# Kernel tuning notes

Hardware: AMD Instinct MI355X
Metric: run time of the kernel (lower is better)

Reference implementation:

```python
import jax, jax.numpy as jnp
import numpy as np

NU = 60000   # num_users
NI = 40000   # num_items
N = NU + NI  # num_nodes
E = 2000000  # num_edges
F = 128      # feat_dim (user_feat_dim == item_feat_dim)
H = 128      # hidden_dim


def setup_inputs() -> dict:
    key = jax.random.key(0)
    ks = jax.random.split(key, 14)
    s = 0.05
    inp = {
        "x": jax.random.normal(ks[0], (N, F), jnp.float32),
        "edge_index": jax.random.randint(ks[1], (2, E), 0, N, dtype=jnp.int32),
        "node_type": jnp.concatenate([jnp.zeros(NU, jnp.int32), jnp.ones(NI, jnp.int32)]),
        # input projections (Linear stores weight as (out, in))
        "w_user": s * jax.random.normal(ks[2], (H, F), jnp.float32),
        "b_user": jnp.zeros((H,), jnp.float32),
        "w_item": s * jax.random.normal(ks[3], (H, F), jnp.float32),
        "b_item": jnp.zeros((H,), jnp.float32),
        # SAGEConv layer 0: lin_l (aggregated neighbors, with bias), lin_r (root, no bias)
        "w_l0": s * jax.random.normal(ks[4], (H, H), jnp.float32),
        "b_l0": s * jax.random.normal(ks[5], (H,), jnp.float32),
        "w_r0": s * jax.random.normal(ks[6], (H, H), jnp.float32),
        # SAGEConv layer 1
        "w_l1": s * jax.random.normal(ks[7], (H, H), jnp.float32),
        "b_l1": s * jax.random.normal(ks[8], (H,), jnp.float32),
        "w_r1": s * jax.random.normal(ks[9], (H, H), jnp.float32),
    }
    return inp


def _sage_conv(h, src, dst, w_l, b_l, w_r):
    # gather source features, max-aggregate onto destinations (PyG aggr='max')
    msg = h[src]                                          # [E, H]
    agg = jax.ops.segment_max(msg, dst, num_segments=N)   # [N, H], -inf where no in-edges
    agg = jnp.where(jnp.isneginf(agg), 0.0, agg)          # PyG fills empty segments with 0
    return agg @ w_l.T + b_l + h @ w_r.T


def reference(x, edge_index, node_type, w_user, b_user, w_item, b_item,
              w_l0, b_l0, w_r0, w_l1, b_l1, w_r1):
    # node_type is sorted: first NU rows are users, rest are items
    src, dst = edge_index[0], edge_index[1]
    user_h = x[:NU] @ w_user.T + b_user                   # [NU, H]
    item_h = x[NU:] @ w_item.T + b_item                   # [NI, H]
    h = jnp.concatenate([user_h, item_h], axis=0)         # [N, H]
    # layer 0 with residual (dims match) then ReLU; dropout is identity in eval
    h = h + _sage_conv(h, src, dst, w_l0, b_l0, w_r0)
    h = jax.nn.relu(h)
    # layer 1 with residual (no activation after last layer)
    h = h + _sage_conv(h, src, dst, w_l1, b_l1, w_r1)
    return (h[:NU], h[NU:])
```

## Files before the change

### kernel.cpp

```cpp
#include <hip/hip_runtime.h>

#define NUSR 60000
#define NITM 40000
#define NN   100000
#define EE   2000000
#define HD   128

#define BW   512
#define NB   196
#define EPB  8192

using bf16x8   = __attribute__((ext_vector_type(8))) short;
using f32x4    = __attribute__((ext_vector_type(4))) float;
using ushort4t = __attribute__((ext_vector_type(4))) unsigned short;
using ushort2t = __attribute__((ext_vector_type(2))) unsigned short;
using ushort8t = __attribute__((ext_vector_type(8))) unsigned short;
using uint4t   = __attribute__((ext_vector_type(4))) unsigned int;

__device__ __forceinline__ unsigned short f2bf(float f) {
    unsigned int u = __float_as_uint(f);
    u += 0x7FFFu + ((u >> 16) & 1u);
    return (unsigned short)(u >> 16);
}
__device__ __forceinline__ float bf2f(unsigned short s) {
    return __uint_as_float(((unsigned int)s) << 16);
}
__device__ __forceinline__ unsigned short keyof(unsigned short b) {
    return (b & 0x8000u) ? (unsigned short)~b : (unsigned short)(b | 0x8000u);
}
__device__ __forceinline__ unsigned unkey32(unsigned k) {
    unsigned negsel = (~k & 0x80008000u) >> 15;
    return k ^ (0x80008000u | (negsel * 0x7FFFu));
}
__device__ __forceinline__ int swz(int row, int col) {
    return row * HD + (col ^ ((row & 7) << 3));
}
__device__ __forceinline__ ushort8t pkmax8(ushort8t a, ushort8t b) {
    return __builtin_elementwise_max(a, b);
}

__global__ __launch_bounds__(256) void bhist_k(const int* __restrict__ dst,
                                               int* __restrict__ bcnt) {
    __shared__ int h[NB];
    int t = threadIdx.x;
    if (t < NB) h[t] = 0;
    __syncthreads();
    int e0 = blockIdx.x * EPB;
    #pragma unroll 4
    for (int i = t; i < EPB; i += 256) {
        int e = e0 + i;
        if (e < EE) atomicAdd(&h[dst[e] >> 9], 1);
    }
    __syncthreads();
    if (t < NB && h[t]) atomicAdd(&bcnt[t], h[t]);
}

__global__ void bscan_k(const int* __restrict__ bcnt, int* __restrict__ bbase,
                        int* __restrict__ bcur, int* __restrict__ off) {
    __shared__ int s[256];
    int t = threadIdx.x;
    int v = (t < NB) ? bcnt[t] : 0;
    s[t] = v;
    __syncthreads();
    for (int d = 1; d < 256; d <<= 1) {
        int a = (t >= d) ? s[t - d] : 0;
        __syncthreads();
        s[t] += a;
        __syncthreads();
    }
    if (t < NB) { bbase[t] = s[t] - v; bcur[t] = s[t] - v; }
    if (t == NB - 1) { bbase[NB] = s[t]; off[NN] = EE; }
}

__global__ __launch_bounds__(256) void bscatter_k(const int* __restrict__ src,
                                                  const int* __restrict__ dst,
                                                  int* __restrict__ bcur,
                                                  unsigned int* __restrict__ bedge) {
    __shared__ int h[NB], base[NB];
    int t = threadIdx.x;
    if (t < NB) h[t] = 0;
    __syncthreads();
    int e0 = blockIdx.x * EPB;
    #pragma unroll 4
    for (int i = t; i < EPB; i += 256) {
        int e = e0 + i;
        if (e < EE) atomicAdd(&h[dst[e] >> 9], 1);
    }
    __syncthreads();
    if (t < NB) {
        int c = h[t];
        base[t] = c ? atomicAdd(&bcur[t], c) : 0;
        h[t] = 0;
    }
    __syncthreads();
    #pragma unroll 4
    for (int i = t; i < EPB; i += 256) {
        int e = e0 + i;
        if (e < EE) {
            int d = dst[e];
            int b = d >> 9;
            int p = base[b] + atomicAdd(&h[b], 1);
            bedge[p] = ((unsigned)(d - (b << 9)) << 17) | (unsigned)src[e];
        }
    }
}

__global__ __launch_bounds__(512) void bcsr_k(const unsigned int* __restrict__ bedge,
                                              const int* __restrict__ bbase,
                                              int* __restrict__ off,
                                              int* __restrict__ csr) {
    __shared__ int cnt[BW], cur[BW], sc[BW];
    int b = blockIdx.x, t = threadIdx.x;
    int n0 = b * BW;
    int nloc = min(BW, NN - n0);
    cnt[t] = 0;
    __syncthreads();
    int e0 = bbase[b], e1 = bbase[b + 1];
    for (int e = e0 + t; e < e1; e += 512)
        atomicAdd(&cnt[bedge[e] >> 17], 1);
    __syncthreads();
    int v = cnt[t];
    sc[t] = v;
    __syncthreads();
    for (int d = 1; d < BW; d <<= 1) {
        int a = (t >= d) ? sc[t - d] : 0;
        __syncthreads();
        sc[t] += a;
        __syncthreads();
    }
    int excl = sc[t] - v;
    if (t < nloc) { off[n0 + t] = e0 + excl; cur[t] = e0 + excl; }
    __syncthreads();
    for (int e = e0 + t; e < e1; e += 512) {
        unsigned ed = bedge[e];
        int p = atomicAdd(&cur[ed >> 17], 1);
        csr[p] = (int)(ed & 0x1FFFFu);
    }
}

__global__ void cvt6i_k(const float* __restrict__ a0, const float* __restrict__ a1,
                        const float* __restrict__ a2, const float* __restrict__ a3,
                        const float* __restrict__ a4, const float* __restrict__ a5,
                        unsigned short* __restrict__ out) {
    int i = blockIdx.x * 256 + threadIdx.x;
    int m = i >> 14, idx = i & 16383;
    const float* s;
    switch (m) {
        case 0: s = a0; break; case 1: s = a1; break; case 2: s = a2; break;
        case 3: s = a3; break; case 4: s = a4; break; default: s = a5; break;
    }
    float v = s[idx];
    if ((m == 3 || m == 5) && (idx >> 7) == (idx & 127)) v += 1.0f;
    out[i] = f2bf(v);
}

__global__ __launch_bounds__(256) void proj_mfma_k(
    const float* __restrict__ x, const unsigned short* __restrict__ wb,
    const float* __restrict__ bias, unsigned short* __restrict__ hkey,
    int row_base, int nrows) {
    __shared__ unsigned short lw[HD * HD];
    int tid = threadIdx.x;
    #pragma unroll
    for (int it = 0; it < 16; ++it) {
        int flat = (it * 256 + tid) * 4;
        int row = flat >> 7, col = flat & 127;
        *(ushort4t*)&lw[swz(row, col)] = *(const ushort4t*)(wb + flat);
    }
    __syncthreads();
    int lane = tid & 63, w = tid >> 6;
    int l15 = lane & 15, l4 = lane >> 4;
    int m0 = blockIdx.x * 128 + w * 32;
    f32x4 acc[2][8] = {};
    #pragma unroll
    for (int kb = 0; kb < 4; ++kb) {
        bf16x8 a[2];
        #pragma unroll
        for (int rt = 0; rt < 2; ++rt) {
            int r = m0 + rt * 16 + l15;
            if (r >= nrows) r = nrows - 1;
            const float* ap = x + (size_t)(row_base + r) * HD + kb * 32 + l4 * 8;
            f32x4 v0 = *(const f32x4*)ap;
            f32x4 v1 = *(const f32x4*)(ap + 4);
            bf16x8 f;
            #pragma unroll
            for (int j = 0; j < 4; ++j) { f[j] = (short)f2bf(v0[j]); f[j + 4] = (short)f2bf(v1[j]); }
            a[rt] = f;
        }
        #pragma unroll
        for (int ct = 0; ct < 8; ++ct) {
            bf16x8 b = *(const bf16x8*)&lw[swz(ct * 16 + l15, kb * 32 + l4 * 8)];
            acc[0][ct] = __builtin_amdgcn_mfma_f32_16x16x32_bf16(a[0], b, acc[0][ct], 0, 0, 0);
            acc[1][ct] = __builtin_amdgcn_mfma_f32_16x16x32_bf16(a[1], b, acc[1][ct], 0, 0, 0);
        }
    }
    __syncthreads();
    #pragma unroll
    for (int ct = 0; ct < 8; ++ct) {
        int col = ct * 16 + l15;
        float bv = bias[col];
        #pragma unroll
        for (int rt = 0; rt < 2; ++rt)
            #pragma unroll
            for (int j = 0; j < 4; ++j) {
                int lrow = w * 32 + rt * 16 + l4 * 4 + j;
                lw[lrow * HD + ((col + ((lrow & 15) << 3)) & 127)] =
                    keyof(f2bf(acc[rt][ct][j] + bv));
            }
    }
    __syncthreads();
    int row = tid >> 1, cb = (tid & 1) * 64;
    int r = blockIdx.x * 128 + row;
    if (r < nrows) {
        int sof = (row & 15) << 3;
        #pragma unroll
        for (int gg = 0; gg < 8; ++gg) {
            uint4t v = *(const uint4t*)&lw[row * HD + ((cb + gg * 8 + sof) & 127)];
            *(uint4t*)(hkey + (size_t)(row_base + r) * HD + cb + gg * 8) = v;
        }
    }
}

__global__ __launch_bounds__(256) void agg_key_k(
    const uint4t* __restrict__ hkey4,
    const int* __restrict__ off, const int* __restrict__ csr,
    uint4t* __restrict__ agg4) {
    int node = (blockIdx.x * 256 + threadIdx.x) >> 6;
    int lane = threadIdx.x & 63;
    if (node >= NN) return;
    int s0 = off[node], s1 = off[node + 1];
    int deg = s1 - s0;
    int q = lane >> 4, l16 = lane & 15;
    ushort8t m = {0, 0, 0, 0, 0, 0, 0, 0};
    int cval = (lane < deg) ? csr[s0 + lane] : 0;
    int nslots = deg < 64 ? deg : 64;
    int niter = (nslots + 3) >> 2;
    for (int u = 0; u < niter; ++u) {
        int idx = u * 4 + q;
        int r = __shfl(cval, idx, 64);
        if (idx < nslots) {
            uint4t v = hkey4[(size_t)r * 16 + l16];
            m = pkmax8(m, *(ushort8t*)&v);
        }
    }
    for (int base = s0 + 64; base < s1; base += 32) {
        #pragma unroll
        for (int u = 0; u < 8; ++u) {
            int jj = base + u * 4 + q;
            if (jj < s1) {
                int r = csr[jj];
                uint4t v = hkey4[(size_t)r * 16 + l16];
                m = pkmax8(m, *(ushort8t*)&v);
            }
        }
    }
    uint4t mu = *(uint4t*)&m;
    #pragma unroll
    for (int c = 0; c < 4; ++c) {
        unsigned a = mu[c];
        unsigned b = (unsigned)__shfl_xor((int)a, 16, 64);
        ushort2t pa = *(ushort2t*)&a, pb = *(ushort2t*)&b;
        pa = __builtin_elementwise_max(pa, pb);
        a = *(unsigned*)&pa;
        b = (unsigned)__shfl_xor((int)a, 32, 64);
        pb = *(ushort2t*)&b;
        pa = __builtin_elementwise_max(pa, pb);
        mu[c] = *(unsigned*)&pa;
    }
    if (q == 0) {
        uint4t outv = {0, 0, 0, 0};
        if (deg > 0) {
            #pragma unroll
            for (int c = 0; c < 4; ++c) outv[c] = unkey32(mu[c]);
        }
        agg4[(size_t)node * 16 + l16] = outv;
    }
}

__global__ __launch_bounds__(512) void combine_mfma_k(
    const unsigned short* __restrict__ hkey, const unsigned short* __restrict__ aggb,
    const unsigned short* __restrict__ wlb, const float* __restrict__ bl,
    const unsigned short* __restrict__ wrb,
    unsigned short* __restrict__ hkey_out, float* __restrict__ fout, int relu) {
    __shared__ unsigned short lw[2][HD * HD];
    int tid = threadIdx.x;
    #pragma unroll
    for (int it = 0; it < 8; ++it) {
        int flat = (it * 512 + tid) * 4;
        int row = flat >> 7, col = flat & 127;
        *(ushort4t*)&lw[0][swz(row, col)] = *(const ushort4t*)(wlb + flat);
        *(ushort4t*)&lw[1][swz(row, col)] = *(const ushort4t*)(wrb + flat);
    }
    __syncthreads();
    int lane = tid & 63, w = tid >> 6;
    int l15 = lane & 15, l4 = lane >> 4;
    int m0 = blockIdx.x * 256 + w * 32;
    const uint4t* hk4 = (const uint4t*)hkey;
    f32x4 acc[2][8] = {};
    #pragma unroll
    for (int kb = 0; kb < 4; ++kb) {
        bf16x8 a1[2], a2[2];
        #pragma unroll
        for (int rt = 0; rt < 2; ++rt) {
            int r = m0 + rt * 16 + l15;
            if (r >= NN) r = NN - 1;
            size_t o = (size_t)r * HD + kb * 32 + l4 * 8;
            a1[rt] = *(const bf16x8*)(aggb + o);
            uint4t aw = hk4[(size_t)r * 16 + kb * 4 + l4];
            bf16x8 f;
            #pragma unroll
            for (int u = 0; u < 4; ++u) {
                unsigned d = unkey32(aw[u]);
                f[2 * u]     = (short)(d & 0xFFFFu);
                f[2 * u + 1] = (short)(d >> 16);
            }
            a2[rt] = f;
        }
        #pragma unroll
        for (int ct = 0; ct < 8; ++ct) {
            bf16x8 b1 = *(const bf16x8*)&lw[0][swz(ct * 16 + l15, kb * 32 + l4 * 8)];
            bf16x8 b2 = *(const bf16x8*)&lw[1][swz(ct * 16 + l15, kb * 32 + l4 * 8)];
            acc[0][ct] = __builtin_amdgcn_mfma_f32_16x16x32_bf16(a1[0], b1, acc[0][ct], 0, 0, 0);
            acc[0][ct] = __builtin_amdgcn_mfma_f32_16x16x32_bf16(a2[0], b2, acc[0][ct], 0, 0, 0);
            acc[1][ct] = __builtin_amdgcn_mfma_f32_16x16x32_bf16(a1[1], b1, acc[1][ct], 0, 0, 0);
            acc[1][ct] = __builtin_amdgcn_mfma_f32_16x16x32_bf16(a2[1], b2, acc[1][ct], 0, 0, 0);
        }
    }
    __syncthreads();
    float* cs = (float*)lw;
    for (int p = 0; p < 2; ++p) {
        if ((w >> 2) == p) {
            #pragma unroll
            for (int ct = 0; ct < 8; ++ct)
                #pragma unroll
                for (int rt = 0; rt < 2; ++rt)
                    #pragma unroll
                    for (int j = 0; j < 4; ++j) {
                        int lrow = (w & 3) * 32 + rt * 16 + l4 * 4 + j;
                        int col = ct * 16 + l15;
                        cs[lrow * HD + ((col + lrow * 4) & 127)] = acc[rt][ct][j];
                    }
        }
        __syncthreads();
        int lrow = tid >> 2, cq = (tid & 3) * 32;
        int r = blockIdx.x * 256 + p * 128 + lrow;
        if (r < NN) {
            const float* crow = cs + lrow * HD;
            int rot = lrow * 4;
            #pragma unroll
            for (int gg = 0; gg < 4; ++gg) {
                int c0 = cq + gg * 8;
                f32x4 cv0 = *(const f32x4*)&crow[(c0 + rot) & 127];
                f32x4 cv1 = *(const f32x4*)&crow[(c0 + 4 + rot) & 127];
                f32x4 bv0 = *(const f32x4*)(bl + c0);
                f32x4 bv1 = *(const f32x4*)(bl + c0 + 4);
                float v[8];
                #pragma unroll
                for (int u = 0; u < 4; ++u) { v[u] = cv0[u] + bv0[u]; v[u + 4] = cv1[u] + bv1[u]; }
                if (relu) {
                    #pragma unroll
                    for (int u = 0; u < 8; ++u) v[u] = fmaxf(v[u], 0.0f);
                }
                if (fout) {
                    f32x4 o0 = {v[0], v[1], v[2], v[3]};
                    f32x4 o1 = {v[4], v[5], v[6], v[7]};
                    *(f32x4*)(fout + (size_t)r * HD + c0) = o0;
                    *(f32x4*)(fout + (size_t)r * HD + c0 + 4) = o1;
                } else {
                    uint4t ov;
                    #pragma unroll
                    for (int u = 0; u < 4; ++u)
                        ov[u] = (unsigned)keyof(f2bf(v[2 * u]))
                              | ((unsigned)keyof(f2bf(v[2 * u + 1])) << 16);
                    *(uint4t*)(hkey_out + (size_t)r * HD + c0) = ov;
                }
            }
        }
        __syncthreads();
    }
}

extern "C" void kernel_launch(void* const* d_in, const int* in_sizes, int n_in,
                              void* d_out, int out_size, void* d_ws, size_t ws_size,
                              hipStream_t stream) {
    const float* x      = (const float*)d_in[0];
    const int*   ei     = (const int*)d_in[1];
    const float* w_user = (const float*)d_in[3];
    const float* b_user = (const float*)d_in[4];
    const float* w_item = (const float*)d_in[5];
    const float* b_item = (const float*)d_in[6];
    const float* w_l0   = (const float*)d_in[7];
    const float* b_l0   = (const float*)d_in[8];
    const float* w_r0   = (const float*)d_in[9];
    const float* w_l1   = (const float*)d_in[10];
    const float* b_l1   = (const float*)d_in[11];
    const float* w_r1   = (const float*)d_in[12];

    const int* e_src = ei;
    const int* e_dst = ei + EE;

    char* ws = (char*)d_ws;
    size_t cur_off = 0;
    auto carve = [&](size_t bytes) {
        void* p = ws + cur_off;
        cur_off = (cur_off + bytes + 255) & ~(size_t)255;
        return p;
    };
    unsigned short* hkey0 = (unsigned short*)carve((size_t)NN * HD * 2);
    unsigned short* hkey1 = (unsigned short*)carve((size_t)NN * HD * 2);
    unsigned short* aggb  = (unsigned short*)carve((size_t)NN * HD * 2);
    unsigned short* wb    = (unsigned short*)carve((size_t)6 * HD * HD * 2);
    int*      off   = (int*)carve((size_t)(NN + 1) * 4);
    int*      csr   = (int*)carve((size_t)EE * 4);
    unsigned* bedge = (unsigned*)carve((size_t)EE * 4);
    int*      bcnt  = (int*)carve((NB + 1) * 4);
    int*      bbase = (int*)carve((NB + 1) * 4);
    int*      bcur  = (int*)carve((NB + 1) * 4);
    (void)ws_size;

    hipMemsetAsync(bcnt, 0, (size_t)NB * 4, stream);
    int nbB = (EE + EPB - 1) / EPB;
    bhist_k<<<nbB, 256, 0, stream>>>(e_dst, bcnt);
    bscan_k<<<1, 256, 0, stream>>>(bcnt, bbase, bcur, off);
    bscatter_k<<<nbB, 256, 0, stream>>>(e_src, e_dst, bcur, bedge);
    bcsr_k<<<NB, 512, 0, stream>>>(bedge, bbase, off, csr);

    cvt6i_k<<<(6 * HD * HD) / 256, 256, 0, stream>>>(w_user, w_item, w_l0, w_r0, w_l1, w_r1, wb);

    proj_mfma_k<<<(NUSR + 127) / 128, 256, 0, stream>>>(x, wb,         b_user, hkey0, 0,    NUSR);
    proj_mfma_k<<<(NITM + 127) / 128, 256, 0, stream>>>(x, wb + 16384, b_item, hkey0, NUSR, NITM);

    agg_key_k<<<NN / 4, 256, 0, stream>>>((const uint4t*)hkey0, off, csr, (uint4t*)aggb);
    combine_mfma_k<<<(NN + 255) / 256, 512, 0, stream>>>(
        hkey0, aggb, wb + 2 * 16384, b_l0, wb + 3 * 16384, hkey1, nullptr, 1);

    agg_key_k<<<NN / 4, 256, 0, stream>>>((const uint4t*)hkey1, off, csr, (uint4t*)aggb);
    combine_mfma_k<<<(NN + 255) / 256, 512, 0, stream>>>(
        hkey1, aggb, wb + 4 * 16384, b_l1, wb + 5 * 16384, nullptr, (float*)d_out, 0);
}
```

Before: 305.4 us.

## Precompute per-block bucket offsets and write fp32 output directly from MFMA registers

The histogram kernel now saves each block's per-bucket counts, and a new per-bucket prefix kernel turns them into exact per-block write bases. The scatter kernel therefore no longer re-reads dst to rebuild the histogram or takes global atomics on bucket cursors. The final combine kernel writes fp32 output straight from accumulator registers, skipping the shared-memory staging pass and its barriers. In exchange there is one extra small launch, and the direct writes are scalar and strided per lane, so they coalesce less well than the staged vector stores.

```diff
diff --git a/kernel.cpp b/kernel.cpp
--- a/kernel.cpp
+++ b/kernel.cpp
@@ -9,6 +9,7 @@
 #define BW   512
 #define NB   196
 #define EPB  8192
+#define NBLK 245
 
 using bf16x8   = __attribute__((ext_vector_type(8))) short;
 using f32x4    = __attribute__((ext_vector_type(4))) float;
@@ -40,6 +41,7 @@
 }
 
 __global__ __launch_bounds__(256) void bhist_k(const int* __restrict__ dst,
+                                               int* __restrict__ gh,
                                                int* __restrict__ bcnt) {
     __shared__ int h[NB];
     int t = threadIdx.x;
@@ -52,11 +54,14 @@
         if (e < EE) atomicAdd(&h[dst[e] >> 9], 1);
     }
     __syncthreads();
-    if (t < NB && h[t]) atomicAdd(&bcnt[t], h[t]);
+    if (t < NB) {
+        gh[blockIdx.x * NB + t] = h[t];
+        if (h[t]) atomicAdd(&bcnt[t], h[t]);
+    }
 }
 
 __global__ void bscan_k(const int* __restrict__ bcnt, int* __restrict__ bbase,
-                        int* __restrict__ bcur, int* __restrict__ off) {
+                        int* __restrict__ off) {
     __shared__ int s[256];
     int t = threadIdx.x;
     int v = (t < NB) ? bcnt[t] : 0;
@@ -68,31 +73,34 @@
         s[t] += a;
         __syncthreads();
     }
-    if (t < NB) { bbase[t] = s[t] - v; bcur[t] = s[t] - v; }
+    if (t < NB) bbase[t] = s[t] - v;
     if (t == NB - 1) { bbase[NB] = s[t]; off[NN] = EE; }
+}
+
+__global__ void bprefix_k(int* __restrict__ gh, const int* __restrict__ bbase) {
+    __shared__ int s[256];
+    int bin = blockIdx.x, t = threadIdx.x;
+    int v = (t < NBLK) ? gh[t * NB + bin] : 0;
+    s[t] = v;
+    __syncthreads();
+    for (int d = 1; d < 256; d <<= 1) {
+        int a = (t >= d) ? s[t - d] : 0;
+        __syncthreads();
+        s[t] += a;
+        __syncthreads();
+    }
+    if (t < NBLK) gh[t * NB + bin] = bbase[bin] + s[t] - v;
 }
 
 __global__ __launch_bounds__(256) void bscatter_k(const int* __restrict__ src,
                                                   const int* __restrict__ dst,
-                                                  int* __restrict__ bcur,
+                                                  const int* __restrict__ gh,
                                                   unsigned int* __restrict__ bedge) {
     __shared__ int h[NB], base[NB];
     int t = threadIdx.x;
-    if (t < NB) h[t] = 0;
+    if (t < NB) { base[t] = gh[blockIdx.x * NB + t]; h[t] = 0; }
     __syncthreads();
     int e0 = blockIdx.x * EPB;
-    #pragma unroll 4
-    for (int i = t; i < EPB; i += 256) {
-        int e = e0 + i;
-        if (e < EE) atomicAdd(&h[dst[e] >> 9], 1);
-    }
-    __syncthreads();
-    if (t < NB) {
-        int c = h[t];
-        base[t] = c ? atomicAdd(&bcur[t], c) : 0;
-        h[t] = 0;
-    }
-    __syncthreads();
     #pragma unroll 4
     for (int i = t; i < EPB; i += 256) {
         int e = e0 + i;
@@ -325,6 +333,25 @@
             acc[1][ct] = __builtin_amdgcn_mfma_f32_16x16x32_bf16(a2[1], b2, acc[1][ct], 0, 0, 0);
         }
     }
+    if (fout) {
+        #pragma unroll
+        for (int ct = 0; ct < 8; ++ct) {
+            int col = ct * 16 + l15;
+            float bv = bl[col];
+            #pragma unroll
+            for (int rt = 0; rt < 2; ++rt)
+                #pragma unroll
+                for (int j = 0; j < 4; ++j) {
+                    int r = m0 + rt * 16 + l4 * 4 + j;
+                    if (r < NN) {
+                        float v = acc[rt][ct][j] + bv;
+                        if (relu) v = fmaxf(v, 0.0f);
+                        fout[(size_t)r * HD + col] = v;
+                    }
+                }
+        }
+        return;
+    }
     __syncthreads();
     float* cs = (float*)lw;
     for (int p = 0; p < 2; ++p) {
@@ -360,19 +387,12 @@
                     #pragma unroll
                     for (int u = 0; u < 8; ++u) v[u] = fmaxf(v[u], 0.0f);
                 }
-                if (fout) {
-                    f32x4 o0 = {v[0], v[1], v[2], v[3]};
-                    f32x4 o1 = {v[4], v[5], v[6], v[7]};
-                    *(f32x4*)(fout + (size_t)r * HD + c0) = o0;
-                    *(f32x4*)(fout + (size_t)r * HD + c0 + 4) = o1;
-                } else {
-                    uint4t ov;
-                    #pragma unroll
-                    for (int u = 0; u < 4; ++u)
-                        ov[u] = (unsigned)keyof(f2bf(v[2 * u]))
-                              | ((unsigned)keyof(f2bf(v[2 * u + 1])) << 16);
-                    *(uint4t*)(hkey_out + (size_t)r * HD + c0) = ov;
-                }
+                uint4t ov;
+                #pragma unroll
+                for (int u = 0; u < 4; ++u)
+                    ov[u] = (unsigned)keyof(f2bf(v[2 * u]))
+                          | ((unsigned)keyof(f2bf(v[2 * u + 1])) << 16);
+                *(uint4t*)(hkey_out + (size_t)r * HD + c0) = ov;
             }
         }
         __syncthreads();
@@ -412,16 +432,16 @@
     int*      off   = (int*)carve((size_t)(NN + 1) * 4);
     int*      csr   = (int*)carve((size_t)EE * 4);
     unsigned* bedge = (unsigned*)carve((size_t)EE * 4);
+    int*      gh    = (int*)carve((size_t)NBLK * NB * 4);
     int*      bcnt  = (int*)carve((NB + 1) * 4);
     int*      bbase = (int*)carve((NB + 1) * 4);
-    int*      bcur  = (int*)carve((NB + 1) * 4);
     (void)ws_size;
 
     hipMemsetAsync(bcnt, 0, (size_t)NB * 4, stream);
-    int nbB = (EE + EPB - 1) / EPB;
-    bhist_k<<<nbB, 256, 0, stream>>>(e_dst, bcnt);
-    bscan_k<<<1, 256, 0, stream>>>(bcnt, bbase, bcur, off);
-    bscatter_k<<<nbB, 256, 0, stream>>>(e_src, e_dst, bcur, bedge);
+    bhist_k<<<NBLK, 256, 0, stream>>>(e_dst, gh, bcnt);
+    bscan_k<<<1, 256, 0, stream>>>(bcnt, bbase, off);
+    bprefix_k<<<NB, 256, 0, stream>>>(gh, bbase);
+    bscatter_k<<<NBLK, 256, 0, stream>>>(e_src, e_dst, gh, bedge);
     bcsr_k<<<NB, 512, 0, stream>>>(bedge, bbase, off, csr);
 
     cvt6i_k<<<(6 * HD * HD) / 256, 256, 0, stream>>>(w_user, w_item, w_l0, w_r0, w_l1, w_r1, wb);
```

After: 290.1 us. 5.0% less time.
